# Kernel optimization log

Hardware: AMD Instinct MI355X
Metric: run time of the kernel (lower is better)

The kernel has to match this reference:

```python
import jax, jax.numpy as jnp
import numpy as np

BS, SL, D = 4, 2048, 1024
H = 16
HD = D // H  # 64


def setup_inputs() -> dict:
    key = jax.random.key(0)
    ks = jax.random.split(key, 11)
    s = 1.0 / np.sqrt(D)
    inp = {
        "value": jax.random.normal(ks[0], (BS, SL, D), jnp.float32),
        "key_in": jax.random.normal(ks[1], (BS, SL, D), jnp.float32),
        "query": jax.random.normal(ks[2], (BS, SL, D), jnp.float32),
        # nn.Linear weights stored [out, in] (torch convention); orthogonal-ish init approximated by scaled normal
        "Wq": jax.random.normal(ks[3], (D, D), jnp.float32) * s,
        "bq": jax.random.normal(ks[4], (D,), jnp.float32) * 0.01,
        "Wk": jax.random.normal(ks[5], (D, D), jnp.float32) * s,
        "bk": jax.random.normal(ks[6], (D,), jnp.float32) * 0.01,
        "Wv": jax.random.normal(ks[7], (D, D), jnp.float32) * s,
        "bv": jax.random.normal(ks[8], (D,), jnp.float32) * 0.01,
        "Wo": jax.random.normal(ks[9], (D, D), jnp.float32) * s,
        "bo": jax.random.normal(ks[10], (D,), jnp.float32) * 0.01,
    }
    return inp


def reference(value, key_in, query, Wq, bq, Wk, bk, Wv, bv, Wo, bo):
    bs, sl, _ = value.shape
    # projections (torch Linear: x @ W.T + b), then split heads -> [b, h, s, hd]
    def proj(x, W, b):
        return (x @ W.T + b).reshape(bs, -1, H, HD).transpose(0, 2, 1, 3)

    q = proj(query, Wq, bq)
    k = proj(key_in, Wk, bk)
    v = proj(value, Wv, bv)

    scale = 1.0 / jnp.sqrt(jnp.asarray(HD, q.dtype))
    logits = jnp.einsum("bhqd,bhkd->bhqk", q, k) * scale  # [b,h,s,s]
    # amax-subtract + softmax == stable softmax
    attn = jax.nn.softmax(logits, axis=-1)
    out = jnp.einsum("bhqk,bhkd->bhqd", attn, v)
    out = out.transpose(0, 2, 1, 3).reshape(bs, sl, D)  # [b,s,D]
    o = out @ Wo.T + bo
    return o
```

## Files before the change

kernel.cpp:

```cpp
#include <hip/hip_runtime.h>
#include <hip/hip_bf16.h>

typedef __bf16 bf16_t;
typedef __bf16 bf16x8 __attribute__((ext_vector_type(8)));
typedef __bf16 bf16x4 __attribute__((ext_vector_type(4)));
typedef float f32x4 __attribute__((ext_vector_type(4)));
typedef float f32x16 __attribute__((ext_vector_type(16)));

#define BS 4
#define SL 2048
#define DM 1024
#define NH 16
#define HD 64

static __device__ __forceinline__ bf16_t tobf(float x) { return (bf16_t)x; }

#if __has_builtin(__builtin_amdgcn_exp2f)
#define EXP2(x) __builtin_amdgcn_exp2f(x)
#else
#define EXP2(x) exp2f(x)
#endif

#if __has_builtin(__builtin_amdgcn_cvt_pk_bf16_f32)
typedef __bf16 bf16x2_t __attribute__((ext_vector_type(2)));
static __device__ __forceinline__ uint32_t pack_bf16(float a, float b) {
  union { bf16x2_t v; uint32_t u; } c;
  c.v = __builtin_amdgcn_cvt_pk_bf16_f32(a, b);
  return c.u;
}
#else
static __device__ __forceinline__ uint32_t pack_bf16(float a, float b) {
  union { bf16_t e[2]; uint32_t u; } c;
  c.e[0] = tobf(a); c.e[1] = tobf(b);
  return c.u;
}
#endif

static __device__ __forceinline__ void glds16(const void* g, void* l) {
  __builtin_amdgcn_global_load_lds(
      (const __attribute__((address_space(1))) void*)g,
      (__attribute__((address_space(3))) void*)l, 16, 0, 0);
}

__global__ void convert_w_kernel(const float* __restrict__ s0, const float* __restrict__ s1,
                                 const float* __restrict__ s2, const float* __restrict__ s3,
                                 bf16_t* __restrict__ d0, bf16_t* __restrict__ d1,
                                 bf16_t* __restrict__ d2, bf16_t* __restrict__ d3)
{
  const float* s; bf16_t* d;
  switch (blockIdx.y) {
    case 0: s = s0; d = d0; break;
    case 1: s = s1; d = d1; break;
    case 2: s = s2; d = d2; break;
    default: s = s3; d = d3; break;
  }
  int i = (blockIdx.x * 256 + threadIdx.x) * 4;
  float4 v = *(const float4*)(s + i);
  bf16x4 o; o[0] = tobf(v.x); o[1] = tobf(v.y); o[2] = tobf(v.z); o[3] = tobf(v.w);
  *(bf16x4*)(d + i) = o;
}

__global__ __launch_bounds__(256, 2) void gemm_qkv_kernel(
    const float* __restrict__ Aq, const float* __restrict__ Ak, const float* __restrict__ Avv,
    const bf16_t* __restrict__ Wcat,
    const float* __restrict__ bq, const float* __restrict__ bk, const float* __restrict__ bvv,
    bf16_t* __restrict__ Qb, bf16_t* __restrict__ Kbo, bf16_t* __restrict__ Vtb)
{
  __shared__ __align__(16) char sMem[49152];

  const int proj = blockIdx.y >> 3;
  const float* Af   = proj == 0 ? Aq : (proj == 1 ? Ak : Avv);
  const float* bias = proj == 0 ? bq : (proj == 1 ? bk : bvv);

  const int tid  = threadIdx.x;
  const int wave = tid >> 6;
  const int lane = tid & 63;
  const int l15  = lane & 15;
  const int quad = lane >> 4;
  const int m0 = blockIdx.x * 128;
  const int nW = blockIdx.y * 128;
  const int n0 = (blockIdx.y & 7) * 128;
  const int wm = (wave & 1) * 64;
  const int wn = (wave >> 1) * 64;

  auto stage = [&](int r, int k0) {
    char* base = sMem + r * 24576;
#pragma unroll
    for (int t = 0; t < 4; t++) {
      int slot = wave * 4 + t;
      int f = slot * 64 + lane;
      int row = f >> 3;
      int cg = (f & 7) ^ (row & 7);
      glds16(Af + (size_t)(m0 + row) * DM + k0 + cg * 4, base + slot * 1024);
    }
#pragma unroll
    for (int t = 0; t < 2; t++) {
      int slot = wave * 2 + t;
      int f = slot * 64 + lane;
      int row = f >> 2;
      int cg = (f & 3) ^ (row & 3);
      glds16(Wcat + (size_t)(nW + row) * DM + k0 + cg * 8, base + 16384 + slot * 1024);
    }
  };

  f32x4 acc[4][4];
#pragma unroll
  for (int i = 0; i < 4; i++)
#pragma unroll
    for (int j = 0; j < 4; j++) acc[i][j] = f32x4{0.f, 0.f, 0.f, 0.f};

  stage(0, 0);
  for (int t = 0; t < 32; ++t) {
    __syncthreads();
    if (t < 31) stage((t + 1) & 1, (t + 1) * 32);

    const float*  sA = (const float*)(sMem + (t & 1) * 24576);
    const bf16_t* sB = (const bf16_t*)(sMem + (t & 1) * 24576 + 16384);

    bf16x8 af[4], bfr[4];
#pragma unroll
    for (int i = 0; i < 4; i++) {
      int row = wm + i * 16 + l15;
      int sw = row & 7;
      const float* base = sA + row * 32;
      f32x4 lo = *(const f32x4*)(base + (((quad * 2)     ^ sw) * 4));
      f32x4 hi = *(const f32x4*)(base + (((quad * 2 + 1) ^ sw) * 4));
      bf16x8 o;
      o[0] = tobf(lo[0]); o[1] = tobf(lo[1]); o[2] = tobf(lo[2]); o[3] = tobf(lo[3]);
      o[4] = tobf(hi[0]); o[5] = tobf(hi[1]); o[6] = tobf(hi[2]); o[7] = tobf(hi[3]);
      af[i] = o;
    }
#pragma unroll
    for (int j = 0; j < 4; j++) {
      int row = wn + j * 16 + l15;
      bfr[j] = *(const bf16x8*)(sB + row * 32 + (quad ^ (row & 3)) * 8);
    }

#pragma unroll
    for (int i = 0; i < 4; i++)
#pragma unroll
      for (int j = 0; j < 4; j++)
        acc[i][j] = __builtin_amdgcn_mfma_f32_16x16x32_bf16(af[i], bfr[j], acc[i][j], 0, 0, 0);
  }

  if (proj < 2) {
    bf16_t* C = proj == 0 ? Qb : Kbo;
#pragma unroll
    for (int j = 0; j < 4; j++) {
      int col = n0 + wn + j * 16 + l15;
      float bv = bias[col];
#pragma unroll
      for (int i = 0; i < 4; i++) {
        int rowb = m0 + wm + i * 16 + quad * 4;
#pragma unroll
        for (int r = 0; r < 4; r++)
          C[(size_t)(rowb + r) * DM + col] = tobf(acc[i][j][r] + bv);
      }
    }
  } else {
#pragma unroll
    for (int j = 0; j < 4; j++) {
      int col = n0 + wn + j * 16 + l15;
      float bv = bias[col];
      int head = col >> 6, hd = col & 63;
#pragma unroll
      for (int i = 0; i < 4; i++) {
        int rowb = m0 + wm + i * 16 + quad * 4;
        int b = rowb >> 11, s = rowb & (SL - 1);
        bf16x4 o;
#pragma unroll
        for (int r = 0; r < 4; r++) o[r] = tobf(acc[i][j][r] + bv);
        *(bf16x4*)(Vtb + ((size_t)(b * NH + head) * HD + hd) * SL + s) = o;
      }
    }
  }
}

__global__ __launch_bounds__(256, 2) void gemm_out_kernel(
    const bf16_t* __restrict__ A, const bf16_t* __restrict__ Bw,
    const float* __restrict__ bias, float* __restrict__ C)
{
  __shared__ __align__(16) char sMem[32768];

  const int tid  = threadIdx.x;
  const int wave = tid >> 6;
  const int lane = tid & 63;
  const int l15  = lane & 15;
  const int quad = lane >> 4;
  const int m0 = blockIdx.x * 128;
  const int n0 = blockIdx.y * 128;
  const int wm = (wave & 1) * 64;
  const int wn = (wave >> 1) * 64;

  auto stage = [&](int r, int k0) {
    char* base = sMem + r * 16384;
#pragma unroll
    for (int t = 0; t < 2; t++) {
      int slot = wave * 2 + t;
      int f = slot * 64 + lane;
      int row = f >> 2;
      int cg = (f & 3) ^ (row & 3);
      glds16(A  + (size_t)(m0 + row) * DM + k0 + cg * 8, base + slot * 1024);
      glds16(Bw + (size_t)(n0 + row) * DM + k0 + cg * 8, base + 8192 + slot * 1024);
    }
  };

  f32x4 acc[4][4];
#pragma unroll
  for (int i = 0; i < 4; i++)
#pragma unroll
    for (int j = 0; j < 4; j++) acc[i][j] = f32x4{0.f, 0.f, 0.f, 0.f};

  stage(0, 0);
  for (int t = 0; t < 32; ++t) {
    __syncthreads();
    if (t < 31) stage((t + 1) & 1, (t + 1) * 32);

    const bf16_t* sA = (const bf16_t*)(sMem + (t & 1) * 16384);
    const bf16_t* sB = sA + 4096;

    bf16x8 af[4], bfr[4];
#pragma unroll
    for (int i = 0; i < 4; i++) {
      int row = wm + i * 16 + l15;
      af[i] = *(const bf16x8*)(sA + row * 32 + (quad ^ (row & 3)) * 8);
    }
#pragma unroll
    for (int j = 0; j < 4; j++) {
      int row = wn + j * 16 + l15;
      bfr[j] = *(const bf16x8*)(sB + row * 32 + (quad ^ (row & 3)) * 8);
    }

#pragma unroll
    for (int i = 0; i < 4; i++)
#pragma unroll
      for (int j = 0; j < 4; j++)
        acc[i][j] = __builtin_amdgcn_mfma_f32_16x16x32_bf16(af[i], bfr[j], acc[i][j], 0, 0, 0);
  }

#pragma unroll
  for (int j = 0; j < 4; j++) {
    int col = n0 + wn + j * 16 + l15;
    float bv = bias[col];
#pragma unroll
    for (int i = 0; i < 4; i++) {
      int rowb = m0 + wm + i * 16 + quad * 4;
#pragma unroll
      for (int r = 0; r < 4; r++)
        C[(size_t)(rowb + r) * DM + col] = acc[i][j][r] + bv;
    }
  }
}

__global__ __launch_bounds__(256, 4) void attn_kernel(
    const bf16_t* __restrict__ Q, const bf16_t* __restrict__ Kb,
    const bf16_t* __restrict__ Vt, bf16_t* __restrict__ O)
{
  __shared__ __align__(16) char sMem[32768];

  const int tid  = threadIdx.x;
  const int wave = tid >> 6;
  const int lane = tid & 63;
  const int l31  = lane & 31;
  const int h    = lane >> 5;
  const int swl  = l31 & 7;

  const int id  = blockIdx.x;
  const int xcd = id & 7, slot = id >> 3;
  const int bh  = xcd * 8 + (slot >> 4);
  const int qi  = slot & 15;
  const int b = bh >> 4, hh = bh & 15;
  const int q0 = qi * 128 + wave * 32;

  auto stage = [&](int r, int k0) {
    char* base = sMem + r * 16384;
#pragma unroll
    for (int t = 0; t < 2; t++) {
      int slot2 = wave * 2 + t;
      int f = slot2 * 64 + lane;
      int row = f >> 3;
      int cg = (f & 7) ^ ((row + (row >> 3)) & 7);
      glds16(Kb + (size_t)(b * SL + k0 + row) * DM + hh * HD + cg * 8,
             base + slot2 * 1024);
      glds16(Vt + ((size_t)bh * HD + row) * SL + k0 + cg * 8,
             base + 8192 + slot2 * 1024);
    }
  };

  bf16x8 qf[4];
  {
    const bf16_t* qp = Q + (size_t)(b * SL + q0 + l31) * DM + hh * HD + h * 8;
#pragma unroll
    for (int c = 0; c < 4; c++) {
      bf16x8 v = *(const bf16x8*)(qp + c * 16);
#pragma unroll
      for (int j = 0; j < 8; j++) v[j] = tobf((float)v[j] * 0.18033688f);
      qf[c] = v;
    }
  }

  f32x16 o_acc[2];
#pragma unroll
  for (int m = 0; m < 2; m++)
#pragma unroll
    for (int r = 0; r < 16; r++) o_acc[m][r] = 0.f;
  float rs0 = 0.f, rs1 = 0.f;

  stage(0, 0);
  for (int t = 0; t < 32; ++t) {
    __syncthreads();
    if (t < 31) stage((t + 1) & 1, (t + 1) * 64);

    const bf16_t* sK = (const bf16_t*)(sMem + (t & 1) * 16384);
    const bf16_t* sV = sK + 4096;

#pragma unroll
    for (int s = 0; s < 2; s++) {
      int rowK = s * 32 + l31;
      int kkK = (rowK + (rowK >> 3)) & 7;
      bf16x8 kf[4];
#pragma unroll
      for (int c = 0; c < 4; c++)
        kf[c] = *(const bf16x8*)(sK + rowK * 64 + (((c * 2 + h) ^ kkK) * 8));

      f32x16 st;
#pragma unroll
      for (int r = 0; r < 16; r++) st[r] = -17.312340f;
#pragma unroll
      for (int c = 0; c < 4; c++)
        st = __builtin_amdgcn_mfma_f32_32x32x16_bf16(kf[c], qf[c], st, 0, 0, 0);

      uint32_t w[8];
#pragma unroll
      for (int i = 0; i < 8; i++) {
        float p0 = EXP2(st[2 * i]);
        float p1 = EXP2(st[2 * i + 1]);
        rs0 += p0; rs1 += p1;
        w[i] = pack_bf16(p0, p1);
      }
      uint32_t y0 = (uint32_t)__shfl_xor((int)(h ? w[0] : w[2]), 32);
      uint32_t y1 = (uint32_t)__shfl_xor((int)(h ? w[1] : w[3]), 32);
      uint32_t y2 = (uint32_t)__shfl_xor((int)(h ? w[4] : w[6]), 32);
      uint32_t y3 = (uint32_t)__shfl_xor((int)(h ? w[5] : w[7]), 32);
      union { uint32_t u[4]; bf16x8 v; } pf0, pf1;
      pf0.u[0] = h ? y0   : w[0];
      pf0.u[1] = h ? y1   : w[1];
      pf0.u[2] = h ? w[2] : y0;
      pf0.u[3] = h ? w[3] : y1;
      pf1.u[0] = h ? y2   : w[4];
      pf1.u[1] = h ? y3   : w[5];
      pf1.u[2] = h ? w[6] : y2;
      pf1.u[3] = h ? w[7] : y3;

#pragma unroll
      for (int m = 0; m < 2; m++) {
        int rowV = m * 32 + l31;
        int kkV = (rowV + (rowV >> 3)) & 7;
#pragma unroll
        for (int c = 0; c < 2; c++) {
          int chunk = (s * 4 + c * 2 + h) ^ kkV;
          bf16x8 vf = *(const bf16x8*)(sV + rowV * 64 + chunk * 8);
          o_acc[m] = __builtin_amdgcn_mfma_f32_32x32x16_bf16(
              vf, (c ? pf1.v : pf0.v), o_acc[m], 0, 0, 0);
        }
      }
    }
  }

  float rs = rs0 + rs1;
  rs += __shfl_xor(rs, 32);
  float inv = 1.f / rs;
  bf16_t* so = (bf16_t*)sMem + wave * 2048;
#pragma unroll
  for (int m = 0; m < 2; m++) {
#pragma unroll
    for (int r = 0; r < 16; r++) {
      int hd = m * 32 + (r & 3) + 8 * (r >> 2) + 4 * h;
      so[l31 * 64 + (((hd >> 3) ^ swl) * 8) + (hd & 7)] = tobf(o_acc[m][r] * inv);
    }
  }
  asm volatile("s_waitcnt lgkmcnt(0)" ::: "memory");
  {
    int qr = lane >> 1, hf = lane & 1;
    int sw2 = qr & 7;
#pragma unroll
    for (int cc = 0; cc < 4; cc++) {
      int chunk = (hf * 4 + cc) ^ sw2;
      bf16x8 v = *(const bf16x8*)(so + qr * 64 + chunk * 8);
      *(bf16x8*)(O + (size_t)(b * SL + q0 + qr) * DM + hh * HD + hf * 32 + cc * 8) = v;
    }
  }
}

extern "C" void kernel_launch(void* const* d_in, const int* in_sizes, int n_in,
                              void* d_out, int out_size, void* d_ws, size_t ws_size,
                              hipStream_t stream)
{
  const float* value  = (const float*)d_in[0];
  const float* key_in = (const float*)d_in[1];
  const float* query  = (const float*)d_in[2];
  const float* Wq = (const float*)d_in[3];
  const float* bq = (const float*)d_in[4];
  const float* Wk = (const float*)d_in[5];
  const float* bk = (const float*)d_in[6];
  const float* Wv = (const float*)d_in[7];
  const float* bv = (const float*)d_in[8];
  const float* Wo = (const float*)d_in[9];
  const float* bo = (const float*)d_in[10];

  char* ws = (char*)d_ws;
  const size_t sz  = (size_t)BS * SL * DM * sizeof(bf16_t);
  const size_t wsz = (size_t)DM * DM * sizeof(bf16_t);
  bf16_t* Qb   = (bf16_t*)(ws + 0 * sz);
  bf16_t* Kb   = (bf16_t*)(ws + 1 * sz);
  bf16_t* Ob   = (bf16_t*)(ws + 2 * sz);
  bf16_t* Vtb  = (bf16_t*)(ws + 3 * sz);
  bf16_t* Wcat = (bf16_t*)(ws + 4 * sz);
  bf16_t* Wob  = (bf16_t*)(ws + 4 * sz + 3 * wsz);

  const int M = BS * SL;

  convert_w_kernel<<<dim3(1024, 4), 256, 0, stream>>>(
      Wq, Wk, Wv, Wo, Wcat, Wcat + DM * DM, Wcat + 2 * DM * DM, Wob);

  gemm_qkv_kernel<<<dim3(M / 128, 24), 256, 0, stream>>>(
      query, key_in, value, Wcat, bq, bk, bv, Qb, Kb, Vtb);

  attn_kernel<<<dim3(SL / 128 * BS * NH), 256, 0, stream>>>(Qb, Kb, Vtb, Ob);

  gemm_out_kernel<<<dim3(M / 128, DM / 128), 256, 0, stream>>>(Ob, Wob, bo, (float*)d_out);
}
```

Baseline: 353.5 us.

## Pre-convert activations to bf16, fold Q scale into projection, retile output GEMM

The fp32 query/key/value inputs are now converted to bf16 in a separate pass before the QKV GEMM, so that GEMM stages bf16 tiles with smaller LDS, skips the in-loop fp32-to-bf16 conversion, and can target higher occupancy. The softmax scale is applied in the Q projection epilogue rather than when the attention kernel loads Q. The output GEMM moves to 128x64 tiles with higher occupancy, giving more blocks. In exchange, the extra conversion pass writes and rereads about 48MB of bf16 activations, and the workspace grows to hold the converted copies.

```diff
diff --git a/kernel.cpp b/kernel.cpp
--- a/kernel.cpp
+++ b/kernel.cpp
@@ -12,6 +12,7 @@
 #define DM 1024
 #define NH 16
 #define HD 64
+#define QSCALE 0.18033688f
 
 static __device__ __forceinline__ bf16_t tobf(float x) { return (bf16_t)x; }
 
@@ -42,34 +43,40 @@
       (__attribute__((address_space(3))) void*)l, 16, 0, 0);
 }
 
-__global__ void convert_w_kernel(const float* __restrict__ s0, const float* __restrict__ s1,
-                                 const float* __restrict__ s2, const float* __restrict__ s3,
-                                 bf16_t* __restrict__ d0, bf16_t* __restrict__ d1,
-                                 bf16_t* __restrict__ d2, bf16_t* __restrict__ d3)
+__global__ void convert_kernel(
+    const float* __restrict__ q, const float* __restrict__ k, const float* __restrict__ v,
+    const float* __restrict__ wq, const float* __restrict__ wk,
+    const float* __restrict__ wv, const float* __restrict__ wo,
+    bf16_t* __restrict__ aq, bf16_t* __restrict__ ak, bf16_t* __restrict__ av,
+    bf16_t* __restrict__ wcat, bf16_t* __restrict__ wob)
 {
-  const float* s; bf16_t* d;
+  const float* s; bf16_t* d; int n;
   switch (blockIdx.y) {
-    case 0: s = s0; d = d0; break;
-    case 1: s = s1; d = d1; break;
-    case 2: s = s2; d = d2; break;
-    default: s = s3; d = d3; break;
+    case 0: s = q;  d = aq;   n = BS * SL * DM; break;
+    case 1: s = k;  d = ak;   n = BS * SL * DM; break;
+    case 2: s = v;  d = av;   n = BS * SL * DM; break;
+    case 3: s = wq; d = wcat;              n = DM * DM; break;
+    case 4: s = wk; d = wcat + DM * DM;    n = DM * DM; break;
+    case 5: s = wv; d = wcat + 2 * DM * DM; n = DM * DM; break;
+    default: s = wo; d = wob;              n = DM * DM; break;
   }
   int i = (blockIdx.x * 256 + threadIdx.x) * 4;
-  float4 v = *(const float4*)(s + i);
-  bf16x4 o; o[0] = tobf(v.x); o[1] = tobf(v.y); o[2] = tobf(v.z); o[3] = tobf(v.w);
+  if (i >= n) return;
+  float4 x = *(const float4*)(s + i);
+  bf16x4 o; o[0] = tobf(x.x); o[1] = tobf(x.y); o[2] = tobf(x.z); o[3] = tobf(x.w);
   *(bf16x4*)(d + i) = o;
 }
 
-__global__ __launch_bounds__(256, 2) void gemm_qkv_kernel(
-    const float* __restrict__ Aq, const float* __restrict__ Ak, const float* __restrict__ Avv,
+__global__ __launch_bounds__(256, 4) void gemm_qkv_kernel(
+    const bf16_t* __restrict__ Aq, const bf16_t* __restrict__ Ak, const bf16_t* __restrict__ Avv,
     const bf16_t* __restrict__ Wcat,
     const float* __restrict__ bq, const float* __restrict__ bk, const float* __restrict__ bvv,
     bf16_t* __restrict__ Qb, bf16_t* __restrict__ Kbo, bf16_t* __restrict__ Vtb)
 {
-  __shared__ __align__(16) char sMem[49152];
+  __shared__ __align__(16) char sMem[32768];
 
   const int proj = blockIdx.y >> 3;
-  const float* Af   = proj == 0 ? Aq : (proj == 1 ? Ak : Avv);
+  const bf16_t* Af  = proj == 0 ? Aq : (proj == 1 ? Ak : Avv);
   const float* bias = proj == 0 ? bq : (proj == 1 ? bk : bvv);
 
   const int tid  = threadIdx.x;
@@ -84,22 +91,15 @@
   const int wn = (wave >> 1) * 64;
 
   auto stage = [&](int r, int k0) {
-    char* base = sMem + r * 24576;
-#pragma unroll
-    for (int t = 0; t < 4; t++) {
-      int slot = wave * 4 + t;
-      int f = slot * 64 + lane;
-      int row = f >> 3;
-      int cg = (f & 7) ^ (row & 7);
-      glds16(Af + (size_t)(m0 + row) * DM + k0 + cg * 4, base + slot * 1024);
-    }
+    char* base = sMem + r * 16384;
 #pragma unroll
     for (int t = 0; t < 2; t++) {
       int slot = wave * 2 + t;
       int f = slot * 64 + lane;
       int row = f >> 2;
       int cg = (f & 3) ^ (row & 3);
-      glds16(Wcat + (size_t)(nW + row) * DM + k0 + cg * 8, base + 16384 + slot * 1024);
+      glds16(Af   + (size_t)(m0 + row) * DM + k0 + cg * 8, base + slot * 1024);
+      glds16(Wcat + (size_t)(nW + row) * DM + k0 + cg * 8, base + 8192 + slot * 1024);
     }
   };
 
@@ -114,21 +114,14 @@
     __syncthreads();
     if (t < 31) stage((t + 1) & 1, (t + 1) * 32);
 
-    const float*  sA = (const float*)(sMem + (t & 1) * 24576);
-    const bf16_t* sB = (const bf16_t*)(sMem + (t & 1) * 24576 + 16384);
+    const bf16_t* sA = (const bf16_t*)(sMem + (t & 1) * 16384);
+    const bf16_t* sB = sA + 4096;
 
     bf16x8 af[4], bfr[4];
 #pragma unroll
     for (int i = 0; i < 4; i++) {
       int row = wm + i * 16 + l15;
-      int sw = row & 7;
-      const float* base = sA + row * 32;
-      f32x4 lo = *(const f32x4*)(base + (((quad * 2)     ^ sw) * 4));
-      f32x4 hi = *(const f32x4*)(base + (((quad * 2 + 1) ^ sw) * 4));
-      bf16x8 o;
-      o[0] = tobf(lo[0]); o[1] = tobf(lo[1]); o[2] = tobf(lo[2]); o[3] = tobf(lo[3]);
-      o[4] = tobf(hi[0]); o[5] = tobf(hi[1]); o[6] = tobf(hi[2]); o[7] = tobf(hi[3]);
-      af[i] = o;
+      af[i] = *(const bf16x8*)(sA + row * 32 + (quad ^ (row & 3)) * 8);
     }
 #pragma unroll
     for (int j = 0; j < 4; j++) {
@@ -143,8 +136,7 @@
         acc[i][j] = __builtin_amdgcn_mfma_f32_16x16x32_bf16(af[i], bfr[j], acc[i][j], 0, 0, 0);
   }
 
-  if (proj < 2) {
-    bf16_t* C = proj == 0 ? Qb : Kbo;
+  if (proj == 0) {
 #pragma unroll
     for (int j = 0; j < 4; j++) {
       int col = n0 + wn + j * 16 + l15;
@@ -154,7 +146,20 @@
         int rowb = m0 + wm + i * 16 + quad * 4;
 #pragma unroll
         for (int r = 0; r < 4; r++)
-          C[(size_t)(rowb + r) * DM + col] = tobf(acc[i][j][r] + bv);
+          Qb[(size_t)(rowb + r) * DM + col] = tobf((acc[i][j][r] + bv) * QSCALE);
+      }
+    }
+  } else if (proj == 1) {
+#pragma unroll
+    for (int j = 0; j < 4; j++) {
+      int col = n0 + wn + j * 16 + l15;
+      float bv = bias[col];
+#pragma unroll
+      for (int i = 0; i < 4; i++) {
+        int rowb = m0 + wm + i * 16 + quad * 4;
+#pragma unroll
+        for (int r = 0; r < 4; r++)
+          Kbo[(size_t)(rowb + r) * DM + col] = tobf(acc[i][j][r] + bv);
       }
     }
   } else {
@@ -176,11 +181,11 @@
   }
 }
 
-__global__ __launch_bounds__(256, 2) void gemm_out_kernel(
+__global__ __launch_bounds__(256, 4) void gemm_out_kernel(
     const bf16_t* __restrict__ A, const bf16_t* __restrict__ Bw,
     const float* __restrict__ bias, float* __restrict__ C)
 {
-  __shared__ __align__(16) char sMem[32768];
+  __shared__ __align__(16) char sMem[24576];
 
   const int tid  = threadIdx.x;
   const int wave = tid >> 6;
@@ -188,45 +193,50 @@
   const int l15  = lane & 15;
   const int quad = lane >> 4;
   const int m0 = blockIdx.x * 128;
-  const int n0 = blockIdx.y * 128;
+  const int n0 = blockIdx.y * 64;
   const int wm = (wave & 1) * 64;
-  const int wn = (wave >> 1) * 64;
+  const int wn = (wave >> 1) * 32;
 
   auto stage = [&](int r, int k0) {
-    char* base = sMem + r * 16384;
+    char* base = sMem + r * 12288;
 #pragma unroll
     for (int t = 0; t < 2; t++) {
       int slot = wave * 2 + t;
       int f = slot * 64 + lane;
       int row = f >> 2;
       int cg = (f & 3) ^ (row & 3);
-      glds16(A  + (size_t)(m0 + row) * DM + k0 + cg * 8, base + slot * 1024);
-      glds16(Bw + (size_t)(n0 + row) * DM + k0 + cg * 8, base + 8192 + slot * 1024);
+      glds16(A + (size_t)(m0 + row) * DM + k0 + cg * 8, base + slot * 1024);
+    }
+    {
+      int f = wave * 64 + lane;
+      int row = f >> 2;
+      int cg = (f & 3) ^ (row & 3);
+      glds16(Bw + (size_t)(n0 + row) * DM + k0 + cg * 8, base + 8192 + wave * 1024);
     }
   };
 
-  f32x4 acc[4][4];
+  f32x4 acc[4][2];
 #pragma unroll
   for (int i = 0; i < 4; i++)
 #pragma unroll
-    for (int j = 0; j < 4; j++) acc[i][j] = f32x4{0.f, 0.f, 0.f, 0.f};
+    for (int j = 0; j < 2; j++) acc[i][j] = f32x4{0.f, 0.f, 0.f, 0.f};
 
   stage(0, 0);
   for (int t = 0; t < 32; ++t) {
     __syncthreads();
     if (t < 31) stage((t + 1) & 1, (t + 1) * 32);
 
-    const bf16_t* sA = (const bf16_t*)(sMem + (t & 1) * 16384);
+    const bf16_t* sA = (const bf16_t*)(sMem + (t & 1) * 12288);
     const bf16_t* sB = sA + 4096;
 
-    bf16x8 af[4], bfr[4];
+    bf16x8 af[4], bfr[2];
 #pragma unroll
     for (int i = 0; i < 4; i++) {
       int row = wm + i * 16 + l15;
       af[i] = *(const bf16x8*)(sA + row * 32 + (quad ^ (row & 3)) * 8);
     }
 #pragma unroll
-    for (int j = 0; j < 4; j++) {
+    for (int j = 0; j < 2; j++) {
       int row = wn + j * 16 + l15;
       bfr[j] = *(const bf16x8*)(sB + row * 32 + (quad ^ (row & 3)) * 8);
     }
@@ -234,12 +244,12 @@
 #pragma unroll
     for (int i = 0; i < 4; i++)
 #pragma unroll
-      for (int j = 0; j < 4; j++)
+      for (int j = 0; j < 2; j++)
         acc[i][j] = __builtin_amdgcn_mfma_f32_16x16x32_bf16(af[i], bfr[j], acc[i][j], 0, 0, 0);
   }
 
 #pragma unroll
-  for (int j = 0; j < 4; j++) {
+  for (int j = 0; j < 2; j++) {
     int col = n0 + wn + j * 16 + l15;
     float bv = bias[col];
 #pragma unroll
@@ -291,12 +301,7 @@
   {
     const bf16_t* qp = Q + (size_t)(b * SL + q0 + l31) * DM + hh * HD + h * 8;
 #pragma unroll
-    for (int c = 0; c < 4; c++) {
-      bf16x8 v = *(const bf16x8*)(qp + c * 16);
-#pragma unroll
-      for (int j = 0; j < 8; j++) v[j] = tobf((float)v[j] * 0.18033688f);
-      qf[c] = v;
-    }
+    for (int c = 0; c < 4; c++) qf[c] = *(const bf16x8*)(qp + c * 16);
   }
 
   f32x16 o_acc[2];
@@ -411,22 +416,25 @@
   char* ws = (char*)d_ws;
   const size_t sz  = (size_t)BS * SL * DM * sizeof(bf16_t);
   const size_t wsz = (size_t)DM * DM * sizeof(bf16_t);
-  bf16_t* Qb   = (bf16_t*)(ws + 0 * sz);
-  bf16_t* Kb   = (bf16_t*)(ws + 1 * sz);
-  bf16_t* Ob   = (bf16_t*)(ws + 2 * sz);
-  bf16_t* Vtb  = (bf16_t*)(ws + 3 * sz);
-  bf16_t* Wcat = (bf16_t*)(ws + 4 * sz);
-  bf16_t* Wob  = (bf16_t*)(ws + 4 * sz + 3 * wsz);
+  bf16_t* Aqb  = (bf16_t*)(ws + 0 * sz);
+  bf16_t* Akb  = (bf16_t*)(ws + 1 * sz);
+  bf16_t* Avb  = (bf16_t*)(ws + 2 * sz);
+  bf16_t* Qb   = (bf16_t*)(ws + 3 * sz);
+  bf16_t* Kb   = (bf16_t*)(ws + 4 * sz);
+  bf16_t* Vtb  = (bf16_t*)(ws + 5 * sz);
+  bf16_t* Wcat = (bf16_t*)(ws + 6 * sz);
+  bf16_t* Wob  = (bf16_t*)(ws + 6 * sz + 3 * wsz);
+  bf16_t* Ob   = Aqb;
 
   const int M = BS * SL;
 
-  convert_w_kernel<<<dim3(1024, 4), 256, 0, stream>>>(
-      Wq, Wk, Wv, Wo, Wcat, Wcat + DM * DM, Wcat + 2 * DM * DM, Wob);
+  convert_kernel<<<dim3(M * DM / 1024, 7), 256, 0, stream>>>(
+      query, key_in, value, Wq, Wk, Wv, Wo, Aqb, Akb, Avb, Wcat, Wob);
 
   gemm_qkv_kernel<<<dim3(M / 128, 24), 256, 0, stream>>>(
-      query, key_in, value, Wcat, bq, bk, bv, Qb, Kb, Vtb);
+      Aqb, Akb, Avb, Wcat, bq, bk, bv, Qb, Kb, Vtb);
 
   attn_kernel<<<dim3(SL / 128 * BS * NH), 256, 0, stream>>>(Qb, Kb, Vtb, Ob);
 
-  gemm_out_kernel<<<dim3(M / 128, DM / 128), 256, 0, stream>>>(Ob, Wob, bo, (float*)d_out);
-}
+  gemm_out_kernel<<<dim3(M / 128, DM / 64), 256, 0, stream>>>(Ob, Wob, bo, (float*)d_out);
+}
```

New measurement: 361.1 us. 2.2% more time.
